# Performance work log

Hardware: AMD Instinct MI355X
Metric: run time of the kernel (lower is better)

Reference implementation:

```python
import jax, jax.numpy as jnp
import numpy as np

# ---- problem constants (match init_kwargs / input_specs) ----
N = 10000        # atoms
E = 160000       # edges
G = 16           # graphs in batch
Z = 10           # num_elements
K = 64           # channels (count of 0e in hidden_irreps)
NB = 8           # num_bessel
SH = 9           # (max_ell+1)^2, max_ell=2
HID = 16         # MLP_irreps 16x0e
R_MAX = 5.0
AVG_NEI = 16.0
P = 5            # num_polynomial_cutoff
L_SLICES = ((0, 1, 0), (1, 4, 1), (4, 9, 2))  # (start, end, l) per irrep block


def _sph(u):
    # real spherical harmonics, 'component' normalization, lmax=2 -> 9 comps
    x, y, z = u[:, 0], u[:, 1], u[:, 2]
    s3, s15, s5 = 3.0 ** 0.5, 15.0 ** 0.5, 5.0 ** 0.5
    one = jnp.ones_like(x)
    return jnp.stack([one,
                      s3 * x, s3 * y, s3 * z,
                      s15 * x * y, s15 * y * z,
                      0.5 * s5 * (3.0 * z * z - 1.0),
                      s15 * x * z, 0.5 * s15 * (x * x - y * y)], axis=-1)


def _radial(r):
    # Bessel basis * polynomial cutoff (p=5)
    n = jnp.arange(1, NB + 1, dtype=r.dtype)
    bess = (2.0 / R_MAX) ** 0.5 * jnp.sin(n[None, :] * jnp.pi * r[:, None] / R_MAX) / r[:, None]
    xx = r / R_MAX
    f = (1.0 - 0.5 * (P + 1) * (P + 2) * xx ** P + P * (P + 2) * xx ** (P + 1)
         - 0.5 * P * (P + 1) * xx ** (P + 2)) * (xx < 1.0)
    return bess * f[:, None]


def _total_energy(positions, node_attrs, shifts, atomic_energies, W_embed, W_up,
                  R1, R2, R3, R4, W_out, W_sc, theta, W_mix, w_read0, Wr1, Wr2,
                  edge_index, batch):
    sender, receiver = edge_index[0], edge_index[1]
    vec = positions[receiver] - positions[sender] + shifts          # [E,3]
    r = jnp.sqrt(jnp.sum(vec * vec, axis=-1) + 1e-9)                # [E]
    u = vec / r[:, None]
    sh = _sph(u)                                                     # [E,9]
    edge_feats = _radial(r)                                          # [E,NB]

    node_e0 = node_attrs @ atomic_energies                           # [N]
    energies = jax.ops.segment_sum(node_e0, batch, num_segments=G)   # [G]

    feats = node_attrs @ W_embed                                     # [N,K] scalar feats
    for i in range(2):
        h = feats @ W_up[i]                                          # [N,K]
        xw = jax.nn.silu(edge_feats @ R1[i])
        xw = jax.nn.silu(xw @ R2[i])
        xw = jax.nn.silu(xw @ R3[i])
        rw = xw @ R4[i]                                              # [E,K] TP weights
        # channel-wise tensor product message + scatter to receiver
        m = rw[:, :, None] * h[sender][:, :, None] * sh[:, None, :]  # [E,K,9]
        A = jax.ops.segment_sum(m, receiver, num_segments=N) / AVG_NEI  # [N,K,9]
        A = jnp.concatenate([jnp.einsum('nkc,kj->njc', A[:, :, s:e], W_out[i, l])
                             for (s, e, l) in L_SLICES], axis=-1)    # per-l linear
        sc = jnp.einsum('nk,nz,zkj->nj', feats, node_attrs, W_sc[i])  # residual (0e)
        # symmetric-contraction product block (correlation=3), element-dependent
        a0 = A[:, :, 0]
        w = jnp.einsum('nz,pzk->pnk', node_attrs, theta[i])           # [3,N,K]
        B = (w[0] + w[1] * a0 + w[2] * a0 * a0)[:, :, None] * A      # [N,K,9]
        B = jnp.einsum('nkc,kj->njc', B, W_mix[i])
        B = B.at[:, :, 0].add(sc)
        feats = B[:, :, 0]                                            # invariant part
        if i == 0:
            node_e = feats @ w_read0                                  # linear readout
        else:
            node_e = jax.nn.silu(feats @ Wr1) @ Wr2                   # nonlinear readout
        energies = energies + jax.ops.segment_sum(node_e, batch, num_segments=G)
    return energies                                                   # [G]


def setup_inputs() -> dict:
    key = jax.random.key(0)
    ks = jax.random.split(key, 24)
    positions = jax.random.normal(ks[0], (N, 3), jnp.float32) * 1.5
    elems = jax.random.randint(ks[1], (N,), 0, Z)
    node_attrs = jax.nn.one_hot(elems, Z, dtype=jnp.float32)
    edge_index = jax.random.randint(ks[2], (2, E), 0, N)
    batch = jnp.sort(jax.random.randint(ks[3], (N,), 0, G))
    shifts = jnp.zeros((E, 3), jnp.float32)
    rn = lambda k, sh, s: jax.random.normal(k, sh, jnp.float32) * s
    return {
        'positions': positions, 'node_attrs': node_attrs, 'shifts': shifts,
        'atomic_energies': rn(ks[4], (Z,), 1.0),
        'W_embed': rn(ks[5], (Z, K), Z ** -0.5),
        'W_up': rn(ks[6], (2, K, K), K ** -0.5),
        'R1': rn(ks[7], (2, NB, 64), NB ** -0.5),
        'R2': rn(ks[8], (2, 64, 64), 64 ** -0.5),
        'R3': rn(ks[9], (2, 64, 64), 64 ** -0.5),
        'R4': rn(ks[10], (2, 64, K), 64 ** -0.5),
        'W_out': rn(ks[11], (2, 3, K, K), K ** -0.5),
        'W_sc': rn(ks[12], (2, Z, K, K), (Z * K) ** -0.5),
        'theta': rn(ks[13], (2, 3, Z, K), 0.1),
        'W_mix': rn(ks[14], (2, K, K), K ** -0.5),
        'w_read0': rn(ks[15], (K,), K ** -0.5),
        'Wr1': rn(ks[16], (K, HID), K ** -0.5),
        'Wr2': rn(ks[17], (HID,), HID ** -0.5),
        'edge_index': edge_index, 'batch': batch,
    }


def reference(positions, node_attrs, shifts, atomic_energies, W_embed, W_up,
              R1, R2, R3, R4, W_out, W_sc, theta, W_mix, w_read0, Wr1, Wr2,
              edge_index, batch):
    def energy(pos):
        return _total_energy(pos, node_attrs, shifts, atomic_energies, W_embed, W_up,
                             R1, R2, R3, R4, W_out, W_sc, theta, W_mix,
                             w_read0, Wr1, Wr2, edge_index, batch)
    total_energy, vjp_fn = jax.vjp(energy, positions)
    (g_pos,) = vjp_fn(jnp.ones((G,), positions.dtype))
    forces = -g_pos
    return total_energy, forces
```

## Files before the change

### kernel.cpp

```cpp
#include <hip/hip_runtime.h>
#include <math.h>

#define N_NODES 10000
#define N_EDGES 160000
#define G_SEG 16
#define ZDIM 10
#define KDIM 64
#define NBESS 8
#define HIDR 16
#define RMAXF 5.0f
#define AVG_NEI_F 16.0f
#define TBINS 256
#define ZROW (TBINS+1)
#define LSTR 68

__device__ __forceinline__ float siluf(float x){ float s = 1.0f/(1.0f+expf(-x)); return x*s; }
__device__ __forceinline__ float dsiluf(float x){ float s = 1.0f/(1.0f+expf(-x)); return s*(1.0f + x*(1.0f-s)); }

__device__ __forceinline__ float waveReduce(float v){
  for (int off = 32; off > 0; off >>= 1) v += __shfl_down(v, off);
  return v;
}

__device__ __forceinline__ float rlane(float v, int l){
  return __int_as_float(__builtin_amdgcn_readlane(__float_as_int(v), l));
}

#define GATHER_NODE(NODE, PTR, PACK, IDXEXPR, LOADH, OUT) { \
  int beg_ = PTR[NODE]; int deg_ = PTR[(NODE)+1] - beg_; \
  float a0_=0.f,a1_=0.f,a2_=0.f,a3_=0.f; \
  for (int base_=0; base_<deg_; base_+=64){ \
    int m_ = min(64, deg_-base_); \
    int b_l = ZROW; float f_l = 0.f; int ix_l = 0; \
    if (lane < m_){ \
      int4 pk = PACK[beg_+base_+lane]; \
      float tp_ = __int_as_float(pk.x) * (TBINS/RMAXF); \
      b_l = (int)tp_; f_l = tp_ - (float)b_l; ix_l = IDXEXPR; \
    } \
    int mr_ = (m_ + 7) & ~7; \
    for (int i_=0; i_<mr_; i_+=8){ \
      int b0_=__shfl(b_l,i_),   b1_=__shfl(b_l,i_+1), b2_=__shfl(b_l,i_+2), b3_=__shfl(b_l,i_+3); \
      int b4_=__shfl(b_l,i_+4), b5_=__shfl(b_l,i_+5), b6_=__shfl(b_l,i_+6), b7_=__shfl(b_l,i_+7); \
      float f0_=__shfl(f_l,i_),   f1_=__shfl(f_l,i_+1), f2_=__shfl(f_l,i_+2), f3_=__shfl(f_l,i_+3); \
      float f4_=__shfl(f_l,i_+4), f5_=__shfl(f_l,i_+5), f6_=__shfl(f_l,i_+6), f7_=__shfl(f_l,i_+7); \
      int s0_=__shfl(ix_l,i_),   s1_=__shfl(ix_l,i_+1), s2_=__shfl(ix_l,i_+2), s3_=__shfl(ix_l,i_+3); \
      int s4_=__shfl(ix_l,i_+4), s5_=__shfl(ix_l,i_+5), s6_=__shfl(ix_l,i_+6), s7_=__shfl(ix_l,i_+7); \
      float2 F0_=Ft2[b0_*KDIM+lane]; float h0_=LOADH(s0_); \
      float2 F1_=Ft2[b1_*KDIM+lane]; float h1_=LOADH(s1_); \
      float2 F2_=Ft2[b2_*KDIM+lane]; float h2_=LOADH(s2_); \
      float2 F3_=Ft2[b3_*KDIM+lane]; float h3_=LOADH(s3_); \
      float2 F4_=Ft2[b4_*KDIM+lane]; float h4_=LOADH(s4_); \
      float2 F5_=Ft2[b5_*KDIM+lane]; float h5_=LOADH(s5_); \
      float2 F6_=Ft2[b6_*KDIM+lane]; float h6_=LOADH(s6_); \
      float2 F7_=Ft2[b7_*KDIM+lane]; float h7_=LOADH(s7_); \
      a0_ += (F0_.x + f0_*(F0_.y-F0_.x))*h0_; a1_ += (F1_.x + f1_*(F1_.y-F1_.x))*h1_; \
      a2_ += (F2_.x + f2_*(F2_.y-F2_.x))*h2_; a3_ += (F3_.x + f3_*(F3_.y-F3_.x))*h3_; \
      a0_ += (F4_.x + f4_*(F4_.y-F4_.x))*h4_; a1_ += (F5_.x + f5_*(F5_.y-F5_.x))*h5_; \
      a2_ += (F6_.x + f6_*(F6_.y-F6_.x))*h6_; a3_ += (F7_.x + f7_*(F7_.y-F7_.x))*h7_; \
    } } \
  OUT = ((a0_+a1_)+(a2_+a3_)); }

#define STAGE3(W0P, W1P, W2P) { \
  for (int idx_ = tid; idx_ < KDIM*KDIM; idx_ += 512){ \
    int r_ = idx_ >> 6, c_ = idx_ & 63; \
    smW[0][r_*LSTR + c_] = (W0P)[idx_]; \
    smW[1][r_*LSTR + c_] = (W1P)[idx_]; \
    smW[2][r_*LSTR + c_] = (W2P)[idx_]; \
  } \
  __syncthreads(); }

#define MVLDS(XV, M, OUT) { \
  const float* Lr_ = &smW[M][lane*LSTR]; \
  float m0_=0.f,m1_=0.f,m2_=0.f,m3_=0.f; \
  _Pragma("unroll") \
  for (int kq_=0; kq_<KDIM/4; kq_++){ \
    float4 mm_ = *(const float4*)&Lr_[4*kq_]; \
    m0_ += rlane(XV,4*kq_+0)*mm_.x; \
    m1_ += rlane(XV,4*kq_+1)*mm_.y; \
    m2_ += rlane(XV,4*kq_+2)*mm_.z; \
    m3_ += rlane(XV,4*kq_+3)*mm_.w; \
  } \
  OUT = (m0_+m1_)+(m2_+m3_); }

#define MVTROW(XV, MT, ROW, OUT) { \
  const float4* Mr_ = (const float4*)((MT) + (ROW)*KDIM); \
  float m0a_=0.f,m1a_=0.f,m2a_=0.f,m3a_=0.f; \
  _Pragma("unroll") \
  for (int kq_=0; kq_<KDIM/4; kq_++){ \
    float4 mm_ = Mr_[kq_]; \
    m0a_ += rlane(XV,4*kq_+0)*mm_.x; \
    m1a_ += rlane(XV,4*kq_+1)*mm_.y; \
    m2a_ += rlane(XV,4*kq_+2)*mm_.z; \
    m3a_ += rlane(XV,4*kq_+3)*mm_.w; \
  } \
  OUT = (m0a_+m1a_)+(m2a_+m3a_); }
#define MVT(XV, MT, OUT) MVTROW(XV, MT, lane, OUT)

#define LOADH_PLAIN(S) rows[(S)*KDIM + lane]
#define LOADH_G2(S)    gAr2c[(S)*KDIM + lane].x

#define NTABW 514
#define SETUP_BASE 333
#define NSETUP (SETUP_BASE + (NTABW+3)/4)

__global__ __launch_bounds__(256) void k_setup(
    const float* We, const float* Wup, const float* Wsc,
    const float* Wout, const float* Wmix,
    const float* Wr1,
    const float* attrs, const float* aE,
    const float* R1g, const float* R2g, const float* R3g, const float* R4g,
    float* M0, float* Msc0,
    float* WoT0, float* WoT1, float* WmixT0, float* WupT1, float* WmixT1,
    float* P1T, float* QtabT, float* WscT1, float* Wr1T,
    float2* Ft2_0, float2* Ft2_1, float* dF4f,
    int* z_buf, float* e_node){
  int blk = blockIdx.x, tid = threadIdx.x;
  const float* Wmix1 = Wmix + KDIM*KDIM;
  const float* Wsc1  = Wsc + ZDIM*KDIM*KDIM;
  if (blk < 5){
    int idx = blk*256 + tid;
    if (idx < 1280){
      int which = idx >= 640;
      int t = which ? idx - 640 : idx;
      int z = t >> 6, j = t & 63;
      float acc = 0.f;
      if (!which){
        #pragma unroll 8
        for (int k = 0; k < KDIM; k++) acc += We[z*KDIM + k] * Wup[k*KDIM + j];
        M0[z*KDIM + j] = acc;
      } else {
        #pragma unroll 8
        for (int k = 0; k < KDIM; k++) acc += We[z*KDIM + k] * Wsc[(z*KDIM + k)*KDIM + j];
        Msc0[z*KDIM + j] = acc;
      }
    }
  } else if (blk < 85){
    int t = (blk-5)*256 + tid;
    int arr = t >> 12;
    int rem = t & 4095;
    int j = rem >> 6, k = rem & 63;
    float v; float* dst;
    switch(arr){
      case 0: v = Wout[k*KDIM + j];                 dst = WoT0;   break;
      case 1: v = Wout[3*KDIM*KDIM + k*KDIM + j];   dst = WoT1;   break;
      case 2: v = Wmix[k*KDIM + j];                 dst = WmixT0; break;
      case 3: v = Wup[KDIM*KDIM + k*KDIM + j];      dst = WupT1;  break;
      default:v = Wmix[KDIM*KDIM + k*KDIM + j];     dst = WmixT1; break;
    }
    dst[rem] = v;
  } else if (blk < 89){
    int t = (blk-85)*256 + tid;
    int h = t >> 6, k = t & 63;
    float acc = 0.f;
    #pragma unroll 8
    for (int j = 0; j < KDIM; j++) acc += Wr1[j*HIDR + h] * Wmix1[k*KDIM + j];
    P1T[k*HIDR + h] = acc;
  } else if (blk < 129){
    int t = (blk-89)*256 + tid;
    int z = t >> 10;
    int rem = t & 1023;
    int h = rem >> 6, k = rem & 63;
    float acc = 0.f;
    #pragma unroll 8
    for (int j = 0; j < KDIM; j++) acc += Wr1[j*HIDR + h] * Wsc1[(z*KDIM + k)*KDIM + j];
    QtabT[(z*KDIM + k)*HIDR + h] = acc;
  } else if (blk < 169){
    int n = (blk-129)*256 + tid;
    if (n < N_NODES){
      int z = 0;
      for (int i = 1; i < ZDIM; i++) if (attrs[n*ZDIM+i] > 0.5f) z = i;
      z_buf[n] = z;
      e_node[n] = aE[z];
    }
  } else if (blk < 329){
    int t = (blk-169)*256 + tid;
    int zz = t >> 12; int rem = t & 4095;
    int j = rem >> 6, k = rem & 63;
    WscT1[(zz*KDIM + j)*KDIM + k] = Wsc1[(zz*KDIM + k)*KDIM + j];
  } else if (blk < SETUP_BASE){
    int t = (blk-329)*256 + tid;
    int h = t >> 6, j = t & 63;
    Wr1T[h*KDIM + j] = Wr1[j*HIDR + h];
  } else {
    int w = tid >> 6, j = tid & 63;
    int wave_id = (blk - SETUP_BASE)*4 + w;
    if (wave_id >= NTABW) return;
    int i = wave_id / (TBINS+1);
    int t = wave_id % (TBINS+1);
    float efv = 0.f, defv = 0.f;
    {
      double r = (double)t * (double)RMAXF / (double)TBINS;
      double wfr = (double)(j+1) * M_PI / (double)RMAXF;
      double c = sqrt(2.0 / (double)RMAXF);
      double bess, dbess;
      if (r < 1e-12){ bess = c*wfr; dbess = 0.0; }
      else {
        double sw = sin(wfr*r), cw = cos(wfr*r);
        bess = c*sw/r;
        dbess = c*(wfr*cw*r - sw)/(r*r);
      }
      double xx = r / (double)RMAXF;
      double f = 0.0, df = 0.0;
      if (xx < 1.0){
        double x2 = xx*xx, x4 = x2*x2, x5 = x4*xx, x6 = x5*xx, x7 = x6*xx;
        f = 1.0 - 21.0*x5 + 35.0*x6 - 15.0*x7;
        df = (-105.0*x4 + 210.0*x5 - 105.0*x6) / (double)RMAXF;
      }
      efv  = (float)(bess*f);
      defv = (float)(dbess*f + bess*df);
    }
    const float* R1 = R1g + i*NBESS*KDIM;
    const float* R2 = R2g + i*KDIM*KDIM;
    const float* R3 = R3g + i*KDIM*KDIM;
    const float* R4 = R4g + i*KDIM*KDIM;
    float z = 0.f, dz = 0.f;
    #pragma unroll
    for (int b = 0; b < NBESS; b++){
      float ef = __shfl(efv, b), def = __shfl(defv, b);
      float wv = R1[b*KDIM+j];
      z += ef*wv; dz += def*wv;
    }
    float v = siluf(z), dv = dsiluf(z)*dz;
    z = 0.f; dz = 0.f;
    for (int k = 0; k < KDIM; k++){
      float xv = __shfl(v, k), dxv = __shfl(dv, k);
      float wv = R2[k*KDIM+j];
      z += xv*wv; dz += dxv*wv;
    }
    float v2 = siluf(z), dv2 = dsiluf(z)*dz;
    z = 0.f; dz = 0.f;
    for (int k = 0; k < KDIM; k++){
      float xv = __shfl(v2, k), dxv = __shfl(dv2, k);
      float wv = R3[k*KDIM+j];
      z += xv*wv; dz += dxv*wv;
    }
    float v3 = siluf(z), dv3 = dsiluf(z)*dz;
    z = 0.f; dz = 0.f;
    for (int k = 0; k < KDIM; k++){
      float xv = __shfl(v3, k), dxv = __shfl(dv3, k);
      float wv = R4[k*KDIM+j];
      z += xv*wv; dz += dxv*wv;
    }
    float2* Ft = i ? Ft2_1 : Ft2_0;
    Ft[t*KDIM+j].x = z;  if (t > 0) Ft[(t-1)*KDIM+j].y = z;
    dF4f[(t*KDIM+j)*4 + 2*i] = dz;
    if (t > 0) dF4f[((t-1)*KDIM+j)*4 + 2*i + 1] = dz;
    if (t == 0) Ft[ZROW*KDIM + j] = make_float2(0.f, 0.f);
  }
}

__global__ __launch_bounds__(256) void k_edge_setup(const float* pos, const float* shifts, const int* ei,
                                                    const int* z_buf,
                                                    float4* evec, int4* emeta,
                                                    int* cnt_r, int* cnt_s){
  int e = blockIdx.x*256 + threadIdx.x;
  int s = ei[e], rcv = ei[N_EDGES + e];
  float dx = pos[rcv*3+0] - pos[s*3+0] + shifts[e*3+0];
  float dy = pos[rcv*3+1] - pos[s*3+1] + shifts[e*3+1];
  float dz = pos[rcv*3+2] - pos[s*3+2] + shifts[e*3+2];
  float r = sqrtf(dx*dx + dy*dy + dz*dz + 1e-9f);
  evec[e] = make_float4(dx, dy, dz, r);
  emeta[e] = make_int4(__float_as_int(r), s, rcv, z_buf[s]);
  if (r < RMAXF){
    atomicAdd(&cnt_s[s], 1);
    atomicAdd(&cnt_r[rcv], 1);
  }
}

__global__ __launch_bounds__(1024) void k_scan(const int* cnt_r, int* ptr_r, int* cur_r,
                                               const int* cnt_s, int* ptr_s, int* cur_s){
  __shared__ int wtot[16];
  __shared__ int woff[16];
  int tid = threadIdx.x;
  int w = tid >> 6, lane = tid & 63;
  const int* cnt = blockIdx.x ? cnt_s : cnt_r;
  int* ptr = blockIdx.x ? ptr_s : ptr_r;
  int* cur = blockIdx.x ? cur_s : cur_r;
  const int per = 10;
  int start = tid*per;
  int csum = 0;
  int cl[per];
  #pragma unroll
  for (int t = 0; t < per; t++){
    int i = start + t;
    int c = (i < N_NODES) ? cnt[i] : 0;
    cl[t] = c; csum += c;
  }
  int v = csum;
  #pragma unroll
  for (int off = 1; off < 64; off <<= 1){
    int u = __shfl_up(v, off);
    if (lane >= off) v += u;
  }
  if (lane == 63) wtot[w] = v;
  __syncthreads();
  if (w == 0 && lane < 16){
    int t = wtot[lane];
    int sv = t;
    #pragma unroll
    for (int off = 1; off < 16; off <<= 1){
      int u = __shfl_up(sv, off);
      if (lane >= off) sv += u;
    }
    woff[lane] = sv - t;
    if (lane == 15) ptr[N_NODES] = sv;
  }
  __syncthreads();
  int run = woff[w] + v - csum;
  #pragma unroll
  for (int t = 0; t < per; t++){
    int i = start + t;
    if (i < N_NODES){ ptr[i] = run; cur[i] = run; run += cl[t]; }
  }
}

__global__ __launch_bounds__(256) void k_fill(const int4* emeta, int* cur_r, int* cur_s,
                                              int4* pr_pack, int4* ps_pack){
  int e = blockIdx.x*256 + threadIdx.x;
  int4 m = emeta[e];
  float r = __int_as_float(m.x);
  if (r >= RMAXF) return;
  int p = atomicAdd(&cur_s[m.y], 1);
  ps_pack[p] = make_int4(m.x, m.z, e, 0);
  int p2 = atomicAdd(&cur_r[m.z], 1);
  pr_pack[p2] = make_int4(m.x, m.y, m.w, e);
}

__global__ __launch_bounds__(512) void k_layer0_fwd(
    const int* z_buf, const int* ptr_r, const int4* pr_pack,
    const float2* Ft2, const float* M0,
    const float* WoT0, const float* WmixT0, const float* WupT1,
    const float* theta0, const float* Msc0, const float* w_read0,
    const float* WscT1,
    float* A0_out, float* h1, float* sc1, float* e_node){
  __shared__ __align__(16) float smW[3][KDIM*LSTR];
  int tid = threadIdx.x;
  int w = tid >> 6, lane = tid & 63;
  STAGE3(WoT0, WmixT0, WupT1)
  int node = blockIdx.x*8 + w;
  int z = z_buf[node];
  const float* rows = M0;
  float acc;
  GATHER_NODE(node, ptr_r, pr_pack, pk.z, LOADH_PLAIN, acc)
  acc *= (1.0f/AVG_NEI_F);
  float a0;
  MVLDS(acc, 0, a0)
  A0_out[node*KDIM+lane] = a0;
  float t0 = theta0[(0*ZDIM+z)*KDIM+lane];
  float t1 = theta0[(1*ZDIM+z)*KDIM+lane];
  float t2 = theta0[(2*ZDIM+z)*KDIM+lane];
  float v = (t0 + t1*a0 + t2*a0*a0)*a0;
  float f;
  MVLDS(v, 1, f)
  f += Msc0[z*KDIM+lane];
  float p = waveReduce(f * w_read0[lane]);
  if (lane == 0) e_node[node] += p;
  float h;
  MVLDS(f, 2, h)
  h1[node*KDIM+lane] = h;
  float s;
  MVT(f, WscT1 + z*KDIM*KDIM, s)
  sc1[node*KDIM+lane] = s;
}

__global__ __launch_bounds__(512) void k_layer1_fwd_bwd(
    const int* z_buf, const int* ptr_r, const int4* pr_pack,
    const float2* Ft2, const float* h1rows,
    const float* WoT1, const float* WmixT1, const float* Wout1raw,
    const float* theta1,
    const float* sc1, const float* Wr1T, const float* Wr2,
    const float* P1T, const float* QtabT, const float* w_read0,
    float2* gAr2, float* gF1, float* e_node){
  __shared__ __align__(16) float smW[3][KDIM*LSTR];
  int tid = threadIdx.x;
  int w = tid >> 6, lane = tid & 63;
  STAGE3(WoT1, WmixT1, Wout1raw)
  int node = blockIdx.x*8 + w;
  int z = z_buf[node];
  const float* rows = h1rows;
  float acc;
  GATHER_NODE(node, ptr_r, pr_pack, pk.y, LOADH_PLAIN, acc)
  acc *= (1.0f/AVG_NEI_F);
  float a0;
  MVLDS(acc, 0, a0)
  float t0 = theta1[(0*ZDIM+z)*KDIM+lane];
  float t1 = theta1[(1*ZDIM+z)*KDIM+lane];
  float t2 = theta1[(2*ZDIM+z)*KDIM+lane];
  float v = (t0 + t1*a0 + t2*a0*a0)*a0;
  float f;
  MVLDS(v, 1, f)
  f += sc1[node*KDIM+lane];
  int hh = lane & 15;
  float tpart;
  MVTROW(f, Wr1T, hh, tpart)
  float wr2 = Wr2[hh];
  float ne = waveReduce(siluf(tpart)*wr2);
  if (lane == 0) e_node[node] += 0.25f*ne;
  float coeff = dsiluf(tpart)*wr2;
  float gP, gs;
  { const float4* Pp_ = (const float4*)(P1T + lane*HIDR);
    const float4* Qp_ = (const float4*)(QtabT + (z*KDIM + lane)*HIDR);
    float pa0_=0.f,pa1_=0.f,pa2_=0.f,pa3_=0.f, qa0_=0.f,qa1_=0.f,qa2_=0.f,qa3_=0.f;
    #pragma unroll
    for (int hq_=0; hq_<HIDR/4; hq_++){
      float4 pm_ = Pp_[hq_]; float4 qm_ = Qp_[hq_];
      float c0_=rlane(coeff,4*hq_+0), c1_=rlane(coeff,4*hq_+1);
      float c2_=rlane(coeff,4*hq_+2), c3_=rlane(coeff,4*hq_+3);
      pa0_ += c0_*pm_.x; pa1_ += c1_*pm_.y; pa2_ += c2_*pm_.z; pa3_ += c3_*pm_.w;
      qa0_ += c0_*qm_.x; qa1_ += c1_*qm_.y; qa2_ += c2_*qm_.z; qa3_ += c3_*qm_.w;
    }
    gP = (pa0_+pa1_)+(pa2_+pa3_); gs = (qa0_+qa1_)+(qa2_+qa3_);
  }
  gF1[node*KDIM+lane] = w_read0[lane] + gs;
  float u = t0 + 2.f*t1*a0 + 3.f*t2*a0*a0;
  float vl = gP*u;
  float gAr;
  MVLDS(vl, 2, gAr)
  gAr2[node*KDIM+lane].x = gAr * (1.0f/AVG_NEI_F);
}

#define NBWD_NODE (N_NODES/8)
#define NBWD_EN   ((N_NODES+511)/512)

__global__ __launch_bounds__(512) void k_bwd_gH0(
    const int* z_buf, const int* ptr_s, const int4* ps_pack,
    const float2* Ft2, const float2* gAr2c,
    const float* Wup1raw, const float* Wmix0raw, const float* Wout0raw,
    const float* gF1,
    const float* A00, const float* theta0,
    const float* e_node, const int* batch, float* out_e,
    float2* gAr2){
  int tid = threadIdx.x;
  if (blockIdx.x >= NBWD_NODE){
    __shared__ float part[G_SEG];
    if (tid < G_SEG) part[tid] = 0.f;
    __syncthreads();
    int n = (blockIdx.x - NBWD_NODE)*512 + tid;
    if (n < N_NODES) atomicAdd(&part[batch[n]], e_node[n]);
    __syncthreads();
    if (tid < G_SEG) atomicAdd(&out_e[tid], part[tid]);
    return;
  }
  __shared__ __align__(16) float smW[3][KDIM*LSTR];
  int w = tid >> 6, lane = tid & 63;
  STAGE3(Wup1raw, Wmix0raw, Wout0raw)
  int node = blockIdx.x*8 + w;
  float ga;
  GATHER_NODE(node, ptr_s, ps_pack, pk.y, LOADH_G2, ga)
  float gfh;
  MVLDS(ga, 0, gfh)
  float gt = gF1[node*KDIM+lane] + gfh;
  float gP;
  MVLDS(gt, 1, gP)
  int z = z_buf[node];
  float a = A00[node*KDIM+lane];
  float t0 = theta0[(0*ZDIM+z)*KDIM+lane];
  float t1 = theta0[(1*ZDIM+z)*KDIM+lane];
  float t2 = theta0[(2*ZDIM+z)*KDIM+lane];
  float u = t0 + 2.f*t1*a + 3.f*t2*a*a;
  float vl = gP*u;
  float gAr;
  MVLDS(vl, 2, gAr)
  gAr2[node*KDIM+lane].y = gAr * (1.0f/AVG_NEI_F);
}

__global__ __launch_bounds__(256) void k_gr(const int4* emeta, const float4* dF4,
                                            const float2* gAr2, const float* h1, const float* M0,
                                            float4* evec){
  int tid = threadIdx.x;
  int e = blockIdx.x*16 + (tid >> 4);
  int li = tid & 15;
  int4 m = emeta[e];
  float r = __int_as_float(m.x);
  if (r >= RMAXF) return;
  float tp = r * (TBINS / RMAXF);
  int b = (int)tp; if (b > TBINS-1) b = TBINS-1;
  float fr = tp - (float)b;
  int k0 = li*4;
  const float4* dp = dF4 + b*KDIM + k0;
  float4 d0 = dp[0], d1 = dp[1], d2 = dp[2], d3 = dp[3];
  const float4* gp = (const float4*)(gAr2 + m.z*KDIM + k0);
  float4 g01 = gp[0], g23 = gp[1];
  float4 hv = *(const float4*)(h1 + m.y*KDIM + k0);
  float4 mv = *(const float4*)(M0 + m.w*KDIM + k0);
  float v;
  v  = g01.x*hv.x*(d0.z + fr*(d0.w-d0.z)) + g01.y*mv.x*(d0.x + fr*(d0.y-d0.x));
  v += g01.z*hv.y*(d1.z + fr*(d1.w-d1.z)) + g01.w*mv.y*(d1.x + fr*(d1.y-d1.x));
  v += g23.x*hv.z*(d2.z + fr*(d2.w-d2.z)) + g23.y*mv.z*(d2.x + fr*(d2.y-d2.x));
  v += g23.z*hv.w*(d3.z + fr*(d3.w-d3.z)) + g23.w*mv.w*(d3.x + fr*(d3.y-d3.x));
  #pragma unroll
  for (int off = 8; off > 0; off >>= 1) v += __shfl_xor(v, off);
  if (li == 0) evec[e].w = v / r;
}

__global__ __launch_bounds__(256) void k_force(const int* ptr_r, const int4* pr_pack,
                                               const int* ptr_s, const int4* ps_pack,
                                               const float4* evec,
                                               float* out_f){
  int tid = threadIdx.x;
  int node = blockIdx.x*16 + (tid >> 4);
  int li = tid & 15;
  float fx=0.f, fy=0.f, fz=0.f;
  int beg = ptr_r[node], end = ptr_r[node+1];
  for (int idx = beg + li; idx < end; idx += 16){
    int e = pr_pack[idx].w;
    float4 ev = evec[e];
    fx -= ev.w*ev.x; fy -= ev.w*ev.y; fz -= ev.w*ev.z;
  }
  beg = ptr_s[node]; end = ptr_s[node+1];
  for (int idx = beg + li; idx < end; idx += 16){
    int e = ps_pack[idx].z;
    float4 ev = evec[e];
    fx += ev.w*ev.x; fy += ev.w*ev.y; fz += ev.w*ev.z;
  }
  #pragma unroll
  for (int off = 8; off > 0; off >>= 1){
    fx += __shfl_xor(fx, off);
    fy += __shfl_xor(fy, off);
    fz += __shfl_xor(fz, off);
  }
  if (li == 0){
    out_f[node*3+0] = fx; out_f[node*3+1] = fy; out_f[node*3+2] = fz;
  }
}

extern "C" void kernel_launch(void* const* d_in, const int* in_sizes, int n_in,
                              void* d_out, int out_size, void* d_ws, size_t ws_size,
                              hipStream_t stream){
  const float* pos    = (const float*)d_in[0];
  const float* attrs  = (const float*)d_in[1];
  const float* shifts = (const float*)d_in[2];
  const float* aE     = (const float*)d_in[3];
  const float* We     = (const float*)d_in[4];
  const float* Wup    = (const float*)d_in[5];
  const float* R1     = (const float*)d_in[6];
  const float* R2     = (const float*)d_in[7];
  const float* R3     = (const float*)d_in[8];
  const float* R4     = (const float*)d_in[9];
  const float* Wout   = (const float*)d_in[10];
  const float* Wsc    = (const float*)d_in[11];
  const float* theta  = (const float*)d_in[12];
  const float* Wmix   = (const float*)d_in[13];
  const float* w_read0= (const float*)d_in[14];
  const float* Wr1    = (const float*)d_in[15];
  const float* Wr2    = (const float*)d_in[16];
  const int*   ei     = (const int*)d_in[17];
  const int*   batch  = (const int*)d_in[18];

  char* base = (char*)d_ws;
  size_t off = 0;
  auto alloc = [&](size_t bytes)->void*{
    void* p = base + off;
    off = (off + bytes + 255) & ~(size_t)255;
    return p;
  };
  float4* evec   = (float4*)alloc(N_EDGES*sizeof(float4));
  int4*   emeta  = (int4*)alloc(N_EDGES*sizeof(int4));
  int4*   pr_pack= (int4*)alloc(N_EDGES*sizeof(int4));
  int4*   ps_pack= (int4*)alloc(N_EDGES*sizeof(int4));
  float*  e_node = (float*)alloc(N_NODES*sizeof(float));
  float*  h1     = (float*)alloc(N_NODES*KDIM*sizeof(float));
  float*  sc1    = (float*)alloc(N_NODES*KDIM*sizeof(float));
  float*  A00    = (float*)alloc(N_NODES*KDIM*sizeof(float));
  float*  gF1    = (float*)alloc(N_NODES*KDIM*sizeof(float));
  float2* gAr2   = (float2*)alloc(N_NODES*KDIM*sizeof(float2));
  float2* Ft2_0  = (float2*)alloc((TBINS+2)*KDIM*sizeof(float2));
  float2* Ft2_1  = (float2*)alloc((TBINS+2)*KDIM*sizeof(float2));
  float4* dF4    = (float4*)alloc((TBINS+1)*KDIM*sizeof(float4));
  float*  M0     = (float*)alloc(ZDIM*KDIM*sizeof(float));
  float*  Msc0   = (float*)alloc(ZDIM*KDIM*sizeof(float));
  float*  WoT0   = (float*)alloc(KDIM*KDIM*sizeof(float));
  float*  WoT1   = (float*)alloc(KDIM*KDIM*sizeof(float));
  float*  WmixT0 = (float*)alloc(KDIM*KDIM*sizeof(float));
  float*  WupT1  = (float*)alloc(KDIM*KDIM*sizeof(float));
  float*  WmixT1 = (float*)alloc(KDIM*KDIM*sizeof(float));
  float*  P1T    = (float*)alloc(KDIM*HIDR*sizeof(float));
  float*  QtabT  = (float*)alloc(ZDIM*KDIM*HIDR*sizeof(float));
  float*  WscT1  = (float*)alloc(ZDIM*KDIM*KDIM*sizeof(float));
  float*  Wr1T   = (float*)alloc(HIDR*KDIM*sizeof(float));
  int* z_buf = (int*)alloc(N_NODES*sizeof(int));
  int* cnt_r = (int*)alloc(N_NODES*sizeof(int));
  int* cnt_s = (int*)alloc(N_NODES*sizeof(int));
  int* ptr_r = (int*)alloc((N_NODES+1)*sizeof(int));
  int* ptr_s = (int*)alloc((N_NODES+1)*sizeof(int));
  int* cur_r = (int*)alloc(N_NODES*sizeof(int));
  int* cur_s = (int*)alloc(N_NODES*sizeof(int));

  float* out_e = (float*)d_out;
  float* out_f = out_e + G_SEG;

  hipMemsetAsync(d_out, 0, (size_t)out_size*sizeof(float), stream);
  hipMemsetAsync(cnt_r, 0, N_NODES*sizeof(int), stream);
  hipMemsetAsync(cnt_s, 0, N_NODES*sizeof(int), stream);

  const int NB8 = N_NODES/8;
  const int EB  = N_EDGES/256;

  const float* Wup1 = Wup + KDIM*KDIM;
  const float* Wout1 = Wout + 3*KDIM*KDIM;
  const float* theta1 = theta + 3*ZDIM*KDIM;

  k_setup<<<NSETUP,256,0,stream>>>(We, Wup, Wsc, Wout, Wmix, Wr1, attrs, aE,
                                   R1, R2, R3, R4,
                                   M0, Msc0, WoT0, WoT1, WmixT0, WupT1, WmixT1,
                                   P1T, QtabT, WscT1, Wr1T,
                                   Ft2_0, Ft2_1, (float*)dF4,
                                   z_buf, e_node);
  k_edge_setup<<<EB,256,0,stream>>>(pos, shifts, ei, z_buf, evec, emeta, cnt_r, cnt_s);
  k_scan<<<2,1024,0,stream>>>(cnt_r, ptr_r, cur_r, cnt_s, ptr_s, cur_s);
  k_fill<<<EB,256,0,stream>>>(emeta, cur_r, cur_s, pr_pack, ps_pack);

  k_layer0_fwd<<<NB8,512,0,stream>>>(z_buf, ptr_r, pr_pack, Ft2_0, M0,
      WoT0, WmixT0, WupT1, theta, Msc0, w_read0, WscT1,
      A00, h1, sc1, e_node);
  k_layer1_fwd_bwd<<<NB8,512,0,stream>>>(z_buf, ptr_r, pr_pack, Ft2_1, h1,
      WoT1, WmixT1, Wout1, theta1, sc1, Wr1T, Wr2,
      P1T, QtabT, w_read0,
      gAr2, gF1, e_node);

  k_bwd_gH0<<<NBWD_NODE + NBWD_EN,512,0,stream>>>(z_buf, ptr_s, ps_pack, Ft2_1, gAr2,
      Wup1, Wmix, Wout, gF1, A00, theta,
      e_node, batch, out_e, gAr2);
  k_gr<<<N_EDGES/16,256,0,stream>>>(emeta, dF4, gAr2, h1, M0, evec);
  k_force<<<N_NODES/16,256,0,stream>>>(ptr_r, pr_pack, ptr_s, ps_pack, evec, out_f);
}
```

Before: 270.7 us.

## Fold mixing matrix into precomputed weight products to remove per-node matvecs

Precomputes products of W_mix with W_up, W_sc and readout weights (Cmu0, WCz, Q2tab, P1H, pv0, bias terms) in setup kernels, so the per-node layer kernels skip the intermediate W_mix matvec in forward and backward. It also stages M0 into shared memory for the layer-0 gather, and replaces the count memsets by zeroing inside k_setup. The extra tail blocks on the edge setup kernel add some setup work and a larger per-z table (WCzT) read from global memory.

```diff
diff --git a/kernel.cpp b/kernel.cpp
--- a/kernel.cpp
+++ b/kernel.cpp
@@ -60,12 +60,11 @@
     } } \
   OUT = ((a0_+a1_)+(a2_+a3_)); }
 
-#define STAGE3(W0P, W1P, W2P) { \
+#define STAGE2(W0P, W1P) { \
   for (int idx_ = tid; idx_ < KDIM*KDIM; idx_ += 512){ \
     int r_ = idx_ >> 6, c_ = idx_ & 63; \
     smW[0][r_*LSTR + c_] = (W0P)[idx_]; \
     smW[1][r_*LSTR + c_] = (W1P)[idx_]; \
-    smW[2][r_*LSTR + c_] = (W2P)[idx_]; \
   } \
   __syncthreads(); }
 
@@ -98,24 +97,27 @@
 
 #define LOADH_PLAIN(S) rows[(S)*KDIM + lane]
 #define LOADH_G2(S)    gAr2c[(S)*KDIM + lane].x
+#define LOADH_M0(S)    smM[(S)*KDIM + lane]
 
 #define NTABW 514
-#define SETUP_BASE 333
+#define SETUP_BASE 302
 #define NSETUP (SETUP_BASE + (NTABW+3)/4)
 
 __global__ __launch_bounds__(256) void k_setup(
     const float* We, const float* Wup, const float* Wsc,
     const float* Wout, const float* Wmix,
-    const float* Wr1,
+    const float* Wr1, const float* w_read0,
     const float* attrs, const float* aE,
     const float* R1g, const float* R2g, const float* R3g, const float* R4g,
     float* M0, float* Msc0,
-    float* WoT0, float* WoT1, float* WmixT0, float* WupT1, float* WmixT1,
-    float* P1T, float* QtabT, float* WscT1, float* Wr1T,
+    float* WoT0, float* WoT1,
+    float* Cmu0R, float* Cmu0T, float* WCzT,
+    float* P1T, float* P1H, float* QtabT, float* Wr1T, float* pv0,
     float2* Ft2_0, float2* Ft2_1, float* dF4f,
-    int* z_buf, float* e_node){
+    int* z_buf, float* e_node, int* cnt_r, int* cnt_s){
   int blk = blockIdx.x, tid = threadIdx.x;
   const float* Wmix1 = Wmix + KDIM*KDIM;
+  const float* Wup1  = Wup + KDIM*KDIM;
   const float* Wsc1  = Wsc + ZDIM*KDIM*KDIM;
   if (blk < 5){
     int idx = blk*256 + tid;
@@ -134,29 +136,39 @@
         Msc0[z*KDIM + j] = acc;
       }
     }
-  } else if (blk < 85){
+  } else if (blk < 37){
     int t = (blk-5)*256 + tid;
     int arr = t >> 12;
     int rem = t & 4095;
     int j = rem >> 6, k = rem & 63;
-    float v; float* dst;
-    switch(arr){
-      case 0: v = Wout[k*KDIM + j];                 dst = WoT0;   break;
-      case 1: v = Wout[3*KDIM*KDIM + k*KDIM + j];   dst = WoT1;   break;
-      case 2: v = Wmix[k*KDIM + j];                 dst = WmixT0; break;
-      case 3: v = Wup[KDIM*KDIM + k*KDIM + j];      dst = WupT1;  break;
-      default:v = Wmix[KDIM*KDIM + k*KDIM + j];     dst = WmixT1; break;
-    }
-    dst[rem] = v;
-  } else if (blk < 89){
-    int t = (blk-85)*256 + tid;
+    if (arr == 0) WoT0[rem] = Wout[k*KDIM + j];
+    else          WoT1[rem] = Wout[3*KDIM*KDIM + k*KDIM + j];
+  } else if (blk < 53){
+    int t = (blk-37)*256 + tid;
+    int r = t >> 6, c = t & 63;
+    float acc = 0.f;
+    #pragma unroll 8
+    for (int k = 0; k < KDIM; k++) acc += Wmix[r*KDIM + k] * Wup1[k*KDIM + c];
+    Cmu0R[r*KDIM + c] = acc;
+    Cmu0T[c*KDIM + r] = acc;
+  } else if (blk < 213){
+    int t = (blk-53)*256 + tid;
+    int z = t >> 12; int rem = t & 4095;
+    int j = rem >> 6, m = rem & 63;
+    float acc = 0.f;
+    #pragma unroll 8
+    for (int k = 0; k < KDIM; k++) acc += Wmix[m*KDIM + k] * Wsc1[(z*KDIM + k)*KDIM + j];
+    WCzT[(z*KDIM + j)*KDIM + m] = acc;
+  } else if (blk < 217){
+    int t = (blk-213)*256 + tid;
     int h = t >> 6, k = t & 63;
     float acc = 0.f;
     #pragma unroll 8
     for (int j = 0; j < KDIM; j++) acc += Wr1[j*HIDR + h] * Wmix1[k*KDIM + j];
     P1T[k*HIDR + h] = acc;
-  } else if (blk < 129){
-    int t = (blk-89)*256 + tid;
+    P1H[h*KDIM + k] = acc;
+  } else if (blk < 257){
+    int t = (blk-217)*256 + tid;
     int z = t >> 10;
     int rem = t & 1023;
     int h = rem >> 6, k = rem & 63;
@@ -164,23 +176,26 @@
     #pragma unroll 8
     for (int j = 0; j < KDIM; j++) acc += Wr1[j*HIDR + h] * Wsc1[(z*KDIM + k)*KDIM + j];
     QtabT[(z*KDIM + k)*HIDR + h] = acc;
-  } else if (blk < 169){
-    int n = (blk-129)*256 + tid;
+  } else if (blk < 297){
+    int n = (blk-257)*256 + tid;
     if (n < N_NODES){
       int z = 0;
       for (int i = 1; i < ZDIM; i++) if (attrs[n*ZDIM+i] > 0.5f) z = i;
       z_buf[n] = z;
       e_node[n] = aE[z];
-    }
-  } else if (blk < 329){
-    int t = (blk-169)*256 + tid;
-    int zz = t >> 12; int rem = t & 4095;
-    int j = rem >> 6, k = rem & 63;
-    WscT1[(zz*KDIM + j)*KDIM + k] = Wsc1[(zz*KDIM + k)*KDIM + j];
-  } else if (blk < SETUP_BASE){
-    int t = (blk-329)*256 + tid;
+      cnt_r[n] = 0; cnt_s[n] = 0;
+    }
+  } else if (blk < 301){
+    int t = (blk-297)*256 + tid;
     int h = t >> 6, j = t & 63;
     Wr1T[h*KDIM + j] = Wr1[j*HIDR + h];
+  } else if (blk < 302){
+    if (tid < KDIM){
+      float acc = 0.f;
+      #pragma unroll 8
+      for (int j = 0; j < KDIM; j++) acc += Wmix[tid*KDIM + j] * w_read0[j];
+      pv0[tid] = acc;
+    }
   } else {
     int w = tid >> 6, j = tid & 63;
     int wave_id = (blk - SETUP_BASE)*4 + w;
@@ -249,11 +264,58 @@
   }
 }
 
+#define EB_MAIN (N_EDGES/256)
+#define EB_TAIL 46
+
 __global__ __launch_bounds__(256) void k_edge_setup(const float* pos, const float* shifts, const int* ei,
                                                     const int* z_buf,
+                                                    const float* Wmix, const float* Wup, const float* Wsc,
+                                                    const float* Msc0, const float* QtabT, const float* w_read0,
+                                                    float* Q2tab, float* biash, float* biass, float* c0z,
                                                     float4* evec, int4* emeta,
                                                     int* cnt_r, int* cnt_s){
-  int e = blockIdx.x*256 + threadIdx.x;
+  int tid = threadIdx.x;
+  if (blockIdx.x >= EB_MAIN){
+    int tb = blockIdx.x - EB_MAIN;
+    const float* Wup1 = Wup + KDIM*KDIM;
+    const float* Wsc1 = Wsc + ZDIM*KDIM*KDIM;
+    if (tb < 40){
+      int idx = tb*256 + tid;
+      int z = idx >> 10; int rem = idx & 1023;
+      int k = rem >> 4, h = rem & 15;
+      float acc = 0.f;
+      #pragma unroll 8
+      for (int j = 0; j < KDIM; j++)
+        acc += Wmix[k*KDIM + j] * QtabT[(z*KDIM + j)*HIDR + h];
+      Q2tab[(z*KDIM + k)*HIDR + h] = acc;
+    } else if (tb < 45){
+      int idx = (tb-40)*256 + tid;
+      if (idx < 1280){
+        int which = idx >= 640;
+        int t = which ? idx - 640 : idx;
+        int z = t >> 6, j = t & 63;
+        float acc = 0.f;
+        if (!which){
+          #pragma unroll 8
+          for (int k = 0; k < KDIM; k++) acc += Msc0[z*KDIM + k] * Wup1[k*KDIM + j];
+          biash[z*KDIM + j] = acc;
+        } else {
+          #pragma unroll 8
+          for (int k = 0; k < KDIM; k++) acc += Msc0[z*KDIM + k] * Wsc1[(z*KDIM + k)*KDIM + j];
+          biass[z*KDIM + j] = acc;
+        }
+      }
+    } else {
+      if (tid < ZDIM){
+        float acc = 0.f;
+        #pragma unroll 8
+        for (int j = 0; j < KDIM; j++) acc += Msc0[tid*KDIM + j] * w_read0[j];
+        c0z[tid] = acc;
+      }
+    }
+    return;
+  }
+  int e = blockIdx.x*256 + tid;
   int s = ei[e], rcv = ei[N_EDGES + e];
   float dx = pos[rcv*3+0] - pos[s*3+0] + shifts[e*3+0];
   float dy = pos[rcv*3+1] - pos[s*3+1] + shifts[e*3+1];
@@ -328,20 +390,26 @@
 
 __global__ __launch_bounds__(512) void k_layer0_fwd(
     const int* z_buf, const int* ptr_r, const int4* pr_pack,
-    const float2* Ft2, const float* M0,
-    const float* WoT0, const float* WmixT0, const float* WupT1,
-    const float* theta0, const float* Msc0, const float* w_read0,
-    const float* WscT1,
+    const float2* Ft2, const float* M0g,
+    const float* WoT0, const float* Cmu0T, const float* WCzT,
+    const float* theta0, const float* biash, const float* biass,
+    const float* pv0, const float* c0z,
     float* A0_out, float* h1, float* sc1, float* e_node){
-  __shared__ __align__(16) float smW[3][KDIM*LSTR];
+  __shared__ __align__(16) float smW[2][KDIM*LSTR];
+  __shared__ float smM[ZDIM*KDIM];
   int tid = threadIdx.x;
   int w = tid >> 6, lane = tid & 63;
-  STAGE3(WoT0, WmixT0, WupT1)
+  for (int idx_ = tid; idx_ < KDIM*KDIM; idx_ += 512){
+    int r_ = idx_ >> 6, c_ = idx_ & 63;
+    smW[0][r_*LSTR + c_] = WoT0[idx_];
+    smW[1][r_*LSTR + c_] = Cmu0T[idx_];
+  }
+  for (int idx_ = tid; idx_ < ZDIM*KDIM; idx_ += 512) smM[idx_] = M0g[idx_];
+  __syncthreads();
   int node = blockIdx.x*8 + w;
   int z = z_buf[node];
-  const float* rows = M0;
   float acc;
-  GATHER_NODE(node, ptr_r, pr_pack, pk.z, LOADH_PLAIN, acc)
+  GATHER_NODE(node, ptr_r, pr_pack, pk.z, LOADH_M0, acc)
   acc *= (1.0f/AVG_NEI_F);
   float a0;
   MVLDS(acc, 0, a0)
@@ -350,31 +418,28 @@
   float t1 = theta0[(1*ZDIM+z)*KDIM+lane];
   float t2 = theta0[(2*ZDIM+z)*KDIM+lane];
   float v = (t0 + t1*a0 + t2*a0*a0)*a0;
-  float f;
-  MVLDS(v, 1, f)
-  f += Msc0[z*KDIM+lane];
-  float p = waveReduce(f * w_read0[lane]);
-  if (lane == 0) e_node[node] += p;
+  float p = waveReduce(v * pv0[lane]);
+  if (lane == 0) e_node[node] += p + c0z[z];
   float h;
-  MVLDS(f, 2, h)
-  h1[node*KDIM+lane] = h;
+  MVLDS(v, 1, h)
+  h1[node*KDIM+lane] = h + biash[z*KDIM+lane];
   float s;
-  MVT(f, WscT1 + z*KDIM*KDIM, s)
-  sc1[node*KDIM+lane] = s;
+  MVT(v, WCzT + z*KDIM*KDIM, s)
+  sc1[node*KDIM+lane] = s + biass[z*KDIM+lane];
 }
 
 __global__ __launch_bounds__(512) void k_layer1_fwd_bwd(
     const int* z_buf, const int* ptr_r, const int4* pr_pack,
     const float2* Ft2, const float* h1rows,
-    const float* WoT1, const float* WmixT1, const float* Wout1raw,
+    const float* WoT1, const float* Wout1raw,
     const float* theta1,
-    const float* sc1, const float* Wr1T, const float* Wr2,
-    const float* P1T, const float* QtabT, const float* w_read0,
+    const float* sc1, const float* P1H, const float* Wr1T, const float* Wr2,
+    const float* P1T, const float* Q2tab, const float* pv0,
     float2* gAr2, float* gF1, float* e_node){
-  __shared__ __align__(16) float smW[3][KDIM*LSTR];
+  __shared__ __align__(16) float smW[2][KDIM*LSTR];
   int tid = threadIdx.x;
   int w = tid >> 6, lane = tid & 63;
-  STAGE3(WoT1, WmixT1, Wout1raw)
+  STAGE2(WoT1, Wout1raw)
   int node = blockIdx.x*8 + w;
   int z = z_buf[node];
   const float* rows = h1rows;
@@ -387,19 +452,19 @@
   float t1 = theta1[(1*ZDIM+z)*KDIM+lane];
   float t2 = theta1[(2*ZDIM+z)*KDIM+lane];
   float v = (t0 + t1*a0 + t2*a0*a0)*a0;
-  float f;
-  MVLDS(v, 1, f)
-  f += sc1[node*KDIM+lane];
+  float scv = sc1[node*KDIM+lane];
   int hh = lane & 15;
-  float tpart;
-  MVTROW(f, Wr1T, hh, tpart)
+  float tpa, tpb;
+  MVTROW(v,   P1H,  hh, tpa)
+  MVTROW(scv, Wr1T, hh, tpb)
+  float tpart = tpa + tpb;
   float wr2 = Wr2[hh];
   float ne = waveReduce(siluf(tpart)*wr2);
   if (lane == 0) e_node[node] += 0.25f*ne;
   float coeff = dsiluf(tpart)*wr2;
-  float gP, gs;
+  float gP, gs2;
   { const float4* Pp_ = (const float4*)(P1T + lane*HIDR);
-    const float4* Qp_ = (const float4*)(QtabT + (z*KDIM + lane)*HIDR);
+    const float4* Qp_ = (const float4*)(Q2tab + (z*KDIM + lane)*HIDR);
     float pa0_=0.f,pa1_=0.f,pa2_=0.f,pa3_=0.f, qa0_=0.f,qa1_=0.f,qa2_=0.f,qa3_=0.f;
     #pragma unroll
     for (int hq_=0; hq_<HIDR/4; hq_++){
@@ -409,13 +474,13 @@
       pa0_ += c0_*pm_.x; pa1_ += c1_*pm_.y; pa2_ += c2_*pm_.z; pa3_ += c3_*pm_.w;
       qa0_ += c0_*qm_.x; qa1_ += c1_*qm_.y; qa2_ += c2_*qm_.z; qa3_ += c3_*qm_.w;
     }
-    gP = (pa0_+pa1_)+(pa2_+pa3_); gs = (qa0_+qa1_)+(qa2_+qa3_);
-  }
-  gF1[node*KDIM+lane] = w_read0[lane] + gs;
+    gP = (pa0_+pa1_)+(pa2_+pa3_); gs2 = (qa0_+qa1_)+(qa2_+qa3_);
+  }
+  gF1[node*KDIM+lane] = pv0[lane] + gs2;
   float u = t0 + 2.f*t1*a0 + 3.f*t2*a0*a0;
   float vl = gP*u;
   float gAr;
-  MVLDS(vl, 2, gAr)
+  MVLDS(vl, 1, gAr)
   gAr2[node*KDIM+lane].x = gAr * (1.0f/AVG_NEI_F);
 }
 
@@ -425,7 +490,7 @@
 __global__ __launch_bounds__(512) void k_bwd_gH0(
     const int* z_buf, const int* ptr_s, const int4* ps_pack,
     const float2* Ft2, const float2* gAr2c,
-    const float* Wup1raw, const float* Wmix0raw, const float* Wout0raw,
+    const float* Cmu0R, const float* Wout0raw,
     const float* gF1,
     const float* A00, const float* theta0,
     const float* e_node, const int* batch, float* out_e,
@@ -441,17 +506,15 @@
     if (tid < G_SEG) atomicAdd(&out_e[tid], part[tid]);
     return;
   }
-  __shared__ __align__(16) float smW[3][KDIM*LSTR];
+  __shared__ __align__(16) float smW[2][KDIM*LSTR];
   int w = tid >> 6, lane = tid & 63;
-  STAGE3(Wup1raw, Wmix0raw, Wout0raw)
+  STAGE2(Cmu0R, Wout0raw)
   int node = blockIdx.x*8 + w;
   float ga;
   GATHER_NODE(node, ptr_s, ps_pack, pk.y, LOADH_G2, ga)
-  float gfh;
-  MVLDS(ga, 0, gfh)
-  float gt = gF1[node*KDIM+lane] + gfh;
-  float gP;
-  MVLDS(gt, 1, gP)
+  float gfm;
+  MVLDS(ga, 0, gfm)
+  float gP = gF1[node*KDIM+lane] + gfm;
   int z = z_buf[node];
   float a = A00[node*KDIM+lane];
   float t0 = theta0[(0*ZDIM+z)*KDIM+lane];
@@ -460,7 +523,7 @@
   float u = t0 + 2.f*t1*a + 3.f*t2*a*a;
   float vl = gP*u;
   float gAr;
-  MVLDS(vl, 2, gAr)
+  MVLDS(vl, 1, gAr)
   gAr2[node*KDIM+lane].y = gAr * (1.0f/AVG_NEI_F);
 }
 
@@ -571,13 +634,18 @@
   float*  Msc0   = (float*)alloc(ZDIM*KDIM*sizeof(float));
   float*  WoT0   = (float*)alloc(KDIM*KDIM*sizeof(float));
   float*  WoT1   = (float*)alloc(KDIM*KDIM*sizeof(float));
-  float*  WmixT0 = (float*)alloc(KDIM*KDIM*sizeof(float));
-  float*  WupT1  = (float*)alloc(KDIM*KDIM*sizeof(float));
-  float*  WmixT1 = (float*)alloc(KDIM*KDIM*sizeof(float));
+  float*  Cmu0R  = (float*)alloc(KDIM*KDIM*sizeof(float));
+  float*  Cmu0T  = (float*)alloc(KDIM*KDIM*sizeof(float));
+  float*  WCzT   = (float*)alloc(ZDIM*KDIM*KDIM*sizeof(float));
   float*  P1T    = (float*)alloc(KDIM*HIDR*sizeof(float));
+  float*  P1H    = (float*)alloc(HIDR*KDIM*sizeof(float));
   float*  QtabT  = (float*)alloc(ZDIM*KDIM*HIDR*sizeof(float));
-  float*  WscT1  = (float*)alloc(ZDIM*KDIM*KDIM*sizeof(float));
+  float*  Q2tab  = (float*)alloc(ZDIM*KDIM*HIDR*sizeof(float));
   float*  Wr1T   = (float*)alloc(HIDR*KDIM*sizeof(float));
+  float*  biash  = (float*)alloc(ZDIM*KDIM*sizeof(float));
+  float*  biass  = (float*)alloc(ZDIM*KDIM*sizeof(float));
+  float*  pv0    = (float*)alloc(KDIM*sizeof(float));
+  float*  c0z    = (float*)alloc(16*sizeof(float));
   int* z_buf = (int*)alloc(N_NODES*sizeof(int));
   int* cnt_r = (int*)alloc(N_NODES*sizeof(int));
   int* cnt_s = (int*)alloc(N_NODES*sizeof(int));
@@ -590,36 +658,36 @@
   float* out_f = out_e + G_SEG;
 
   hipMemsetAsync(d_out, 0, (size_t)out_size*sizeof(float), stream);
-  hipMemsetAsync(cnt_r, 0, N_NODES*sizeof(int), stream);
-  hipMemsetAsync(cnt_s, 0, N_NODES*sizeof(int), stream);
 
   const int NB8 = N_NODES/8;
-  const int EB  = N_EDGES/256;
-
-  const float* Wup1 = Wup + KDIM*KDIM;
+
   const float* Wout1 = Wout + 3*KDIM*KDIM;
   const float* theta1 = theta + 3*ZDIM*KDIM;
 
-  k_setup<<<NSETUP,256,0,stream>>>(We, Wup, Wsc, Wout, Wmix, Wr1, attrs, aE,
+  k_setup<<<NSETUP,256,0,stream>>>(We, Wup, Wsc, Wout, Wmix, Wr1, w_read0, attrs, aE,
                                    R1, R2, R3, R4,
-                                   M0, Msc0, WoT0, WoT1, WmixT0, WupT1, WmixT1,
-                                   P1T, QtabT, WscT1, Wr1T,
+                                   M0, Msc0, WoT0, WoT1,
+                                   Cmu0R, Cmu0T, WCzT,
+                                   P1T, P1H, QtabT, Wr1T, pv0,
                                    Ft2_0, Ft2_1, (float*)dF4,
-                                   z_buf, e_node);
-  k_edge_setup<<<EB,256,0,stream>>>(pos, shifts, ei, z_buf, evec, emeta, cnt_r, cnt_s);
+                                   z_buf, e_node, cnt_r, cnt_s);
+  k_edge_setup<<<EB_MAIN+EB_TAIL,256,0,stream>>>(pos, shifts, ei, z_buf,
+                                   Wmix, Wup, Wsc, Msc0, QtabT, w_read0,
+                                   Q2tab, biash, biass, c0z,
+                                   evec, emeta, cnt_r, cnt_s);
   k_scan<<<2,1024,0,stream>>>(cnt_r, ptr_r, cur_r, cnt_s, ptr_s, cur_s);
-  k_fill<<<EB,256,0,stream>>>(emeta, cur_r, cur_s, pr_pack, ps_pack);
+  k_fill<<<EB_MAIN,256,0,stream>>>(emeta, cur_r, cur_s, pr_pack, ps_pack);
 
   k_layer0_fwd<<<NB8,512,0,stream>>>(z_buf, ptr_r, pr_pack, Ft2_0, M0,
-      WoT0, WmixT0, WupT1, theta, Msc0, w_read0, WscT1,
+      WoT0, Cmu0T, WCzT, theta, biash, biass, pv0, c0z,
       A00, h1, sc1, e_node);
   k_layer1_fwd_bwd<<<NB8,512,0,stream>>>(z_buf, ptr_r, pr_pack, Ft2_1, h1,
-      WoT1, WmixT1, Wout1, theta1, sc1, Wr1T, Wr2,
-      P1T, QtabT, w_read0,
+      WoT1, Wout1, theta1, sc1, P1H, Wr1T, Wr2,
+      P1T, Q2tab, pv0,
       gAr2, gF1, e_node);
 
   k_bwd_gH0<<<NBWD_NODE + NBWD_EN,512,0,stream>>>(z_buf, ptr_s, ps_pack, Ft2_1, gAr2,
-      Wup1, Wmix, Wout, gF1, A00, theta,
+      Cmu0R, Wout, gF1, A00, theta,
       e_node, batch, out_e, gAr2);
   k_gr<<<N_EDGES/16,256,0,stream>>>(emeta, dF4, gAr2, h1, M0, evec);
   k_force<<<N_NODES/16,256,0,stream>>>(ptr_r, pr_pack, ptr_s, ps_pack, evec, out_f);
```

Result: no change. 272.9 us (+0.8%).
